# Kernel tuning notes

Hardware: AMD Instinct MI355X
Metric: run time of the kernel (lower is better)

Reference implementation:

```python
import jax, jax.numpy as jnp
import numpy as np

# dims: F=N_fault, V=N_train (noise samples), E=batch, M=n_in+2, N=n_out
F, V, E, N_IN, N_OUT = 2, 4, 2048, 512, 512
M = N_IN + 2
GMIN, GMAX, EPS_TRAIN, PGMIN = 0.01, 10.0, 0.1, 1e-4
ETA2_ACT1 = 0.20  # ACT1.eta_fault[0,2], used in theta init
# pTanh activation params per ACT: a = e0 + e1*tanh((z-e2)*e3)
ETAS = np.array([[0.05, 0.90, 0.20, 8.0],
                 [0.10, 0.80, 0.30, 5.0],
                 [0.00, 1.00, 0.25, 10.0],
                 [0.15, 0.70, 0.15, 6.0]], dtype=np.float32)


def setup_inputs() -> dict:
    key = jax.random.key(0)
    k1, k2, k3, k4, k5 = jax.random.split(key, 5)
    a_previous = jax.random.uniform(k1, (F, V, E, N_IN), jnp.float32)
    # theta init per __init__: rand/100 + gmin; last row += gmax; row -2 from eta_2 formula
    theta = jax.random.uniform(k2, (M, N_OUT), jnp.float32) / 100.0 + GMIN
    theta = theta.at[-1, :].add(GMAX)
    theta = theta.at[-2, :].set(ETA2_ACT1 / (1.0 - ETA2_ACT1) * (jnp.sum(theta[:-2, :], 0) + theta[-1, :]))
    cofficients_act = jax.random.uniform(k3, (4, N_OUT), jnp.float32)
    noise_u = jax.random.uniform(k4, (F, V, M, N_OUT), jnp.float32)   # theta_noisy uniform draw
    gumbel_u = jax.random.uniform(k5, (4, N_OUT), jnp.float32)        # gumbel uniform draw
    return {"a_previous": a_previous, "theta_": theta,
            "cofficients_act": cofficients_act, "noise_u": noise_u, "gumbel_u": gumbel_u}


def _forward(a_previous, theta_, cofficients_act, noise_u, gumbel_u):
    sg = jax.lax.stop_gradient
    # --- theta property: clamp to [-gmax,gmax], zero |.|<gmin, straight-through ---
    th_c = jnp.clip(theta_, -GMAX, GMAX)
    th_t = jnp.where(jnp.abs(th_c) < GMIN, 0.0, th_c)
    theta = sg(th_t) + theta_ - sg(theta_)
    # --- theta_noisy: multiplicative uniform noise in [1-eps, 1+eps]; FaultMask == 1 ---
    theta_noisy = theta[None, None] * ((noise_u * 2.0 - 1.0) * EPS_TRAIN + 1.0)  # [F,V,M,N]
    absn = jnp.abs(theta_noisy)
    W = absn / (jnp.sum(absn, axis=2, keepdims=True) + 1e-10)
    pos = (theta_noisy >= 0).astype(theta_noisy.dtype)
    neg = 1.0 - pos
    # --- MAC: extend input with [ones, zeros], inverter path, split-sign matmul ---
    ones = jnp.ones(a_previous.shape[:3] + (1,), a_previous.dtype)
    zeros = jnp.zeros_like(ones)
    x_ext = jnp.concatenate([a_previous, ones, zeros], axis=3)  # [F,V,E,M]
    x_neg = (-x_ext).at[..., -1].set(0.0)                       # ideal INV(a) = -a, last col zeroed
    z = (jnp.einsum('fvem,fvmn->fven', x_ext, W * pos)
         + jnp.einsum('fvem,fvmn->fven', x_neg, W * neg))       # [F,V,E,N]
    # --- MAC_power: vectorized form of the quad loop ---
    # Power = sum_{f,v,m,n} g[m,n] * sum_e (x_ext*pos + x_neg*neg - y)^2 / (E*V*F)
    # pos*neg = 0, pos^2 = pos  =>  expand the square into einsum reductions.
    g_init = jnp.abs(th_c)
    g_tilde = g_init * (PGMIN / jnp.min(g_init, axis=0, keepdims=True))
    pos_d, neg_d = sg(pos), sg(neg)  # detached in torch source
    sx2 = jnp.einsum('fvem,fvem->fvm', x_ext, x_ext)
    sn2 = jnp.einsum('fvem,fvem->fvm', x_neg, x_neg)
    sy2 = jnp.einsum('fven,fven->fvn', z, z)
    C = jnp.einsum('fvem,fven->fvmn', x_ext, z)
    D = jnp.einsum('fvem,fven->fvmn', x_neg, z)
    p1 = (jnp.einsum('fvm,fvmn,mn->', sx2, pos_d, g_tilde)
          + jnp.einsum('fvm,fvmn,mn->', sn2, neg_d, g_tilde))
    p2 = -2.0 * (jnp.einsum('fvmn,fvmn,mn->', C, pos_d, g_tilde)
                 + jnp.einsum('fvmn,fvmn,mn->', D, neg_d, g_tilde))
    p3 = jnp.einsum('fvn,n->', sy2, jnp.sum(g_tilde, axis=0))
    mac_power = (p1 + p2 + p3) / (E * V * F)
    # --- CoFF_ACT: clamped logits + gumbel, softmax, hard argmax straight-through ---
    c = cofficients_act + sg(jnp.clip(cofficients_act, -1.0, 1.0) - cofficients_act)
    gn = -jnp.log(-jnp.log(gumbel_u + 1e-20) + 1e-20)
    alpha = jax.nn.softmax((c + gn) / 1.0, axis=0)              # temperature = 1.0
    hard = jax.nn.one_hot(jnp.argmax(alpha, axis=0), 4, axis=0, dtype=alpha.dtype)
    alpha_st = sg(hard) + alpha - sg(alpha)                      # [4, N]
    # --- mix the four pTanh activations ---
    a_new = jnp.zeros_like(z)
    for i in range(4):
        e0, e1, e2, e3 = ETAS[i]
        a_new = a_new + alpha_st[i] * (e0 + e1 * jnp.tanh((z - e2) * e3))
    return a_new, mac_power


def reference(a_previous, theta_, cofficients_act, noise_u, gumbel_u):
    return _forward(a_previous, theta_, cofficients_act, noise_u, gumbel_u)
```

## Files before the change

kernel.cpp:

```cpp
#include <hip/hip_runtime.h>

typedef unsigned short u16;
typedef __attribute__((ext_vector_type(8))) short short8;
typedef __attribute__((ext_vector_type(4))) float f32x4;

#define NF 2
#define NV 4
#define FV 8
#define NE 2048
#define NIN 512
#define NOUT 512
#define NM 514

#define WS_P1      0u
#define WS_P2      2048u
#define WS_P3      3072u
#define WS_SCALE   4224u
#define WS_G       6272u
#define WS_GN      8448u
#define WS_ETA     10496u
#define WS_BIASZ   18688u
#define WS_BIAST   35072u
#define WS_DENP    51456u
#define WS_PMIN    182528u
#define WS_PSUM    313600u
#define WS_ABF     444672u
#define WS_BZT     17221888u
#define WS_BTT     21416192u

__constant__ float c_etas[4][4] = {
    {0.05f, 0.90f, 0.20f, 8.0f},
    {0.10f, 0.80f, 0.30f, 5.0f},
    {0.00f, 1.00f, 0.25f, 10.0f},
    {0.15f, 0.70f, 0.15f, 6.0f}};

__device__ __forceinline__ u16 f2bf(float x) {
    unsigned u = __float_as_uint(x);
    unsigned r = (u + 0x7fffu + ((u >> 16) & 1u)) >> 16;
    return (u16)r;
}

__device__ __forceinline__ void gll16(const void* g, void* l) {
    __builtin_amdgcn_global_load_lds((__attribute__((address_space(1))) void*)g,
                                     (__attribute__((address_space(3))) void*)l,
                                     16, 0, 0);
}

__global__ void kA_part(const float* __restrict__ theta_, float* __restrict__ pmin,
                        float* __restrict__ psum, float* __restrict__ wszero) {
    int t = threadIdx.x;
    if (blockIdx.x == 0) {
        for (int i = t; i < 1056; i += 256) wszero[i] = 0.f;
    }
    int n2 = t * 2;
    int r0 = blockIdx.x * 9;
    float mn0 = 3.4e38f, mn1 = 3.4e38f, s0 = 0.f, s1 = 0.f;
    int rend = r0 + 9;
    if (rend > NM) rend = NM;
    for (int r = r0; r < rend; r++) {
        float2 v = *(const float2*)(theta_ + r * NOUT + n2);
        float a0 = fabsf(fminf(fmaxf(v.x, -10.f), 10.f));
        float a1 = fabsf(fminf(fmaxf(v.y, -10.f), 10.f));
        mn0 = fminf(mn0, a0); mn1 = fminf(mn1, a1);
        s0 += a0; s1 += a1;
    }
    *(float2*)(pmin + blockIdx.x * NOUT + n2) = make_float2(mn0, mn1);
    *(float2*)(psum + blockIdx.x * NOUT + n2) = make_float2(s0, s1);
}

__global__ void kB_fold(const float* __restrict__ pmin, const float* __restrict__ psum,
                        const float* __restrict__ coeff, const float* __restrict__ gumb,
                        float* __restrict__ scale, float* __restrict__ Gn,
                        float4* __restrict__ eta4) {
    int n = threadIdx.x;
    float mn = 3.4e38f, s = 0.f;
    for (int i = 0; i < 64; i++) {
        mn = fminf(mn, pmin[i * NOUT + n]);
        s += psum[i * NOUT + n];
    }
    float sc = 1e-4f / mn;
    scale[n] = sc;
    Gn[n] = sc * s;
    float best = -1e30f;
    int bi = 0;
    for (int i = 0; i < 4; i++) {
        float c = fminf(fmaxf(coeff[i * NOUT + n], -1.f), 1.f);
        float u = gumb[i * NOUT + n];
        float g = -logf(-logf(u + 1e-20f) + 1e-20f);
        float v = c + g;
        if (v > best) { best = v; bi = i; }
    }
    eta4[n] = make_float4(c_etas[bi][0], c_etas[bi][1], c_etas[bi][2], c_etas[bi][3]);
}

__global__ void kC_grow(const float* __restrict__ theta_, const float* __restrict__ scale,
                        float* __restrict__ G) {
    int m = blockIdx.x;
    int t = threadIdx.x;
    const float4* rowp = (const float4*)(theta_ + m * NOUT);
    const float4* scp = (const float4*)scale;
    float acc = 0.f;
#pragma unroll
    for (int i = 0; i < 2; i++) {
        float4 v = rowp[t * 2 + i];
        float4 s = scp[t * 2 + i];
        acc += fabsf(fminf(fmaxf(v.x, -10.f), 10.f)) * s.x
             + fabsf(fminf(fmaxf(v.y, -10.f), 10.f)) * s.y
             + fabsf(fminf(fmaxf(v.z, -10.f), 10.f)) * s.z
             + fabsf(fminf(fmaxf(v.w, -10.f), 10.f)) * s.w;
    }
    for (int off = 32; off > 0; off >>= 1) acc += __shfl_down(acc, off);
    if (t == 0) G[m] = acc;
}

__global__ void k_wmat3(const float* __restrict__ theta_, const float* __restrict__ scale,
                        const float* __restrict__ noise,
                        u16* __restrict__ BzT, u16* __restrict__ BtT,
                        float* __restrict__ bias_z, float* __restrict__ bias_t,
                        float* __restrict__ denomp) {
    const int nt = blockIdx.x, mt = blockIdx.y, fv = blockIdx.z;
    const int t = threadIdx.x;
    const int nq = t & 15, mr = t >> 4;
    const int nb = nt * 64 + nq * 4;
    __shared__ u16 Wl[64][72];
    __shared__ u16 Sl[64][72];
    __shared__ float4 red[16][17];
    float4 sc4 = *(const float4*)(scale + nb);
    float4 dacc = {0.f, 0.f, 0.f, 0.f};
#pragma unroll
    for (int i = 0; i < 4; i++) {
        int ml = mr + i * 16;
        int m = mt * 64 + ml;
        float4 th4 = *(const float4*)(theta_ + m * NOUT + nb);
        float4 no4 = *(const float4*)(noise + (fv * NM + m) * NOUT + nb);
        ushort4 wv, sv;
#define WCOMP(c, fld) { float fac = no4.c * 0.2f + 0.9f; \
                        float thc = fminf(fmaxf(th4.c, -10.f), 10.f); \
                        float gi = fabsf(thc); \
                        float tht = (gi < 0.01f) ? 0.f : thc; \
                        float th = tht * fac; \
                        wv.fld = f2bf(th); \
                        sv.fld = f2bf(((th >= 0.f) ? gi : -gi) * sc4.c); \
                        dacc.c += fabsf(th); }
        WCOMP(x, x) WCOMP(y, y) WCOMP(z, z) WCOMP(w, w)
#undef WCOMP
        *(ushort4*)(&Wl[ml][nq * 4]) = wv;
        *(ushort4*)(&Sl[ml][nq * 4]) = sv;
    }
    red[mr][nq] = dacc;
    __syncthreads();
    if (t < 16) {
        float4 s = red[0][t];
#pragma unroll
        for (int r = 1; r < 16; r++) {
            float4 v = red[r][t];
            s.x += v.x; s.y += v.y; s.z += v.z; s.w += v.w;
        }
        *(float4*)(denomp + (mt * 8 + fv) * NOUT + nt * 64 + t * 4) = s;
    }
    const int mb = (t & 15) * 4;
#pragma unroll
    for (int r = 0; r < 4; r++) {
        int nl = (t >> 4) + r * 16;
        ushort4 wv, sv;
        wv.x = Wl[mb][nl]; wv.y = Wl[mb + 1][nl]; wv.z = Wl[mb + 2][nl]; wv.w = Wl[mb + 3][nl];
        sv.x = Sl[mb][nl]; sv.y = Sl[mb + 1][nl]; sv.z = Sl[mb + 2][nl]; sv.w = Sl[mb + 3][nl];
        int gidx = (fv * NOUT + nt * 64 + nl) * NIN + mt * 64 + mb;
        *(ushort4*)(BzT + gidx) = wv;
        *(ushort4*)(BtT + gidx) = sv;
    }
    if (mt == 0 && t < 64) {
        int n = nt * 64 + t;
        float fac = noise[(fv * NM + 512) * NOUT + n] * 0.2f + 0.9f;
        float thc = fminf(fmaxf(theta_[512 * NOUT + n], -10.f), 10.f);
        float gi = fabsf(thc);
        float tht = (gi < 0.01f) ? 0.f : thc;
        float th = tht * fac;
        bias_z[fv * NOUT + n] = th;
        bias_t[fv * NOUT + n] = ((th >= 0.f) ? gi : -gi) * scale[n];
    }
}

__global__ void k_prepA(const float* __restrict__ a_prev, const float* __restrict__ G,
                        u16* __restrict__ Abf, float* __restrict__ p1slot) {
    int t = threadIdx.x;
    float acc = 0.f;
#pragma unroll
    for (int i = 0; i < 4; i++) {
        int idx = (i * 2048 + blockIdx.x) * 256 + t;
        float4 v = ((const float4*)a_prev)[idx];
        int k = (idx & 127) << 2;
        float4 g4 = *((const float4*)(G + k));
        acc += v.x * v.x * g4.x + v.y * v.y * g4.y + v.z * v.z * g4.z + v.w * v.w * g4.w;
        ushort4 o;
        o.x = f2bf(v.x); o.y = f2bf(v.y); o.z = f2bf(v.z); o.w = f2bf(v.w);
        ((ushort4*)Abf)[idx] = o;
    }
    for (int off = 32; off > 0; off >>= 1) acc += __shfl_down(acc, off);
    __shared__ float red[4];
    int lane = t & 63, wv = t >> 6;
    if (lane == 0) red[wv] = acc;
    __syncthreads();
    if (t == 0)
        atomicAdd(&p1slot[(blockIdx.x & 63) * 8], red[0] + red[1] + red[2] + red[3]);
}

__global__ __launch_bounds__(256, 2) void k_gemm(
    const u16* __restrict__ Abf, const u16* __restrict__ BzT, const u16* __restrict__ BtT,
    const float* __restrict__ bias_z, const float* __restrict__ bias_t,
    const float* __restrict__ Gn, const float4* __restrict__ eta4,
    const float* __restrict__ theta_, const float* __restrict__ noise,
    const float* __restrict__ denomp,
    float* __restrict__ out, float* __restrict__ p2slot, float* __restrict__ p3slot) {
    __shared__ alignas(16) u16 As[128 * 64];
    __shared__ alignas(16) u16 Bzs[128 * 64];
    __shared__ alignas(16) u16 Bts[128 * 64];
    const int tid = threadIdx.x;
    const int lane = tid & 63;
    const int wv = tid >> 6;
    const int wr = wv >> 1, wc = wv & 1;
    const int b = blockIdx.x;
    const int fv = b & 7;
    const int kk = b >> 3;
    const int n0 = (kk & 3) * 128;
    const int e0 = (kk >> 2) * 128;

    const u16* Ag = Abf + (fv * NE + e0) * NIN;
    const u16* Bzg = BzT + (fv * NOUT + n0) * NIN;
    const u16* Btg = BtT + (fv * NOUT + n0) * NIN;

    f32x4 accz[4][4], acct[4][4];
#pragma unroll
    for (int i = 0; i < 4; i++)
#pragma unroll
        for (int j = 0; j < 4; j++) {
            f32x4 zz = {0.f, 0.f, 0.f, 0.f};
            accz[i][j] = zz;
            acct[i][j] = zz;
        }

    const int srow = tid >> 3;
    const int swz = (((tid & 7) ^ (srow & 7))) * 8;

    for (int k0 = 0; k0 < 512; k0 += 64) {
#pragma unroll
        for (int i = 0; i < 4; i++) {
            int so = (i * 32 + srow) * 512 + k0 + swz;
            int dof = i * 2048 + tid * 8;
            gll16(Ag + so, (u16*)As + dof);
            gll16(Bzg + so, (u16*)Bzs + dof);
            gll16(Btg + so, (u16*)Bts + dof);
        }
        __builtin_amdgcn_s_waitcnt(0);
        __syncthreads();
        const int rA = wr * 64 + (lane & 15);
        const int rB = wc * 64 + (lane & 15);
#pragma unroll
        for (int s = 0; s < 2; s++) {
            const int ca = ((s * 4 + (lane >> 4)) ^ (lane & 7)) * 8;
            short8 af[4], bzf[4], btf[4];
#pragma unroll
            for (int i = 0; i < 4; i++) af[i] = *(const short8*)(As + (rA + i * 16) * 64 + ca);
#pragma unroll
            for (int j = 0; j < 4; j++) {
                bzf[j] = *(const short8*)(Bzs + (rB + j * 16) * 64 + ca);
                btf[j] = *(const short8*)(Bts + (rB + j * 16) * 64 + ca);
            }
#pragma unroll
            for (int i = 0; i < 4; i++)
#pragma unroll
                for (int j = 0; j < 4; j++) {
                    accz[i][j] = __builtin_amdgcn_mfma_f32_16x16x32_bf16(af[i], bzf[j], accz[i][j], 0, 0, 0);
                    acct[i][j] = __builtin_amdgcn_mfma_f32_16x16x32_bf16(af[i], btf[j], acct[i][j], 0, 0, 0);
                }
        }
        __syncthreads();
    }

    float p2 = 0.f, p3 = 0.f;
    const int col = lane & 15;
    const int rowq = (lane >> 4) * 4;
#pragma unroll
    for (int j = 0; j < 4; j++) {
        int n = n0 + wc * 64 + j * 16 + col;
        float dsum = 1e-10f;
#pragma unroll
        for (int mc = 0; mc < 8; mc++) dsum += denomp[(mc * 8 + fv) * NOUT + n];
#pragma unroll
        for (int mx = 512; mx < 514; mx++) {
            float fac = noise[(fv * NM + mx) * NOUT + n] * 0.2f + 0.9f;
            float thc = fminf(fmaxf(theta_[mx * NOUT + n], -10.f), 10.f);
            float tht = (fabsf(thc) < 0.01f) ? 0.f : thc;
            dsum += fabsf(tht * fac);
        }
        float rdv = 1.f / dsum;
        float bz = bias_z[fv * NOUT + n];
        float bt = bias_t[fv * NOUT + n];
        float gnv = Gn[n];
        float4 e4 = eta4[n];
#pragma unroll
        for (int i = 0; i < 4; i++) {
            int ebase = e0 + wr * 64 + i * 16 + rowq;
#pragma unroll
            for (int r = 0; r < 4; r++) {
                float z = (accz[i][j][r] + bz) * rdv;
                float t = acct[i][j][r] + bt;
                p2 += z * t;
                p3 += z * z * gnv;
                float x = (z - e4.z) * e4.w;
                float ex = __expf(2.f * x);
                float th = 1.f - 2.f / (ex + 1.f);
                out[(fv * NE + ebase + r) * NOUT + n] = e4.x + e4.y * th;
            }
        }
    }
    for (int off = 32; off > 0; off >>= 1) {
        p2 += __shfl_down(p2, off);
        p3 += __shfl_down(p3, off);
    }
    __shared__ float r2[4], r3[4];
    if (lane == 0) { r2[wv] = p2; r3[wv] = p3; }
    __syncthreads();
    if (tid == 0) {
        int slot = (b & 31) * 8;
        atomicAdd(&p2slot[slot], r2[0] + r2[1] + r2[2] + r2[3]);
        atomicAdd(&p3slot[slot], r3[0] + r3[1] + r3[2] + r3[3]);
    }
}

__global__ void k_final(const float* __restrict__ p1s, const float* __restrict__ p2s,
                        const float* __restrict__ p3s, const float* __restrict__ G,
                        float* __restrict__ out) {
    int t = threadIdx.x;
    float s1 = p1s[t * 8];
    float s2 = (t < 32) ? p2s[t * 8] : 0.f;
    float s3 = (t < 32) ? p3s[t * 8] : 0.f;
    for (int off = 32; off > 0; off >>= 1) {
        s1 += __shfl_down(s1, off);
        s2 += __shfl_down(s2, off);
        s3 += __shfl_down(s3, off);
    }
    if (t == 0) {
        float mp = (s1 + 16384.f * G[512] - 2.f * s2 + s3) * (1.f / 16384.f);
        out[8388608] = mp;
    }
}

extern "C" void kernel_launch(void* const* d_in, const int* in_sizes, int n_in,
                              void* d_out, int out_size, void* d_ws, size_t ws_size,
                              hipStream_t stream) {
    const float* a_prev = (const float*)d_in[0];
    const float* theta_ = (const float*)d_in[1];
    const float* coeff = (const float*)d_in[2];
    const float* noise = (const float*)d_in[3];
    const float* gumb = (const float*)d_in[4];
    float* out = (float*)d_out;
    char* w = (char*)d_ws;
    float* p1s = (float*)(w + WS_P1);
    float* p2s = (float*)(w + WS_P2);
    float* p3s = (float*)(w + WS_P3);
    float* scale = (float*)(w + WS_SCALE);
    float* G = (float*)(w + WS_G);
    float* Gn = (float*)(w + WS_GN);
    float4* eta4 = (float4*)(w + WS_ETA);
    float* bias_z = (float*)(w + WS_BIASZ);
    float* bias_t = (float*)(w + WS_BIAST);
    float* denomp = (float*)(w + WS_DENP);
    float* pmin = (float*)(w + WS_PMIN);
    float* psum = (float*)(w + WS_PSUM);
    u16* Abf = (u16*)(w + WS_ABF);
    u16* BzT = (u16*)(w + WS_BZT);
    u16* BtT = (u16*)(w + WS_BTT);

    kA_part<<<64, 256, 0, stream>>>(theta_, pmin, psum, (float*)w);
    kB_fold<<<1, 512, 0, stream>>>(pmin, psum, coeff, gumb, scale, Gn, eta4);
    kC_grow<<<514, 64, 0, stream>>>(theta_, scale, G);
    k_wmat3<<<dim3(8, 8, FV), 256, 0, stream>>>(theta_, scale, noise, BzT, BtT,
                                                bias_z, bias_t, denomp);
    k_prepA<<<2048, 256, 0, stream>>>(a_prev, G, Abf, p1s);
    k_gemm<<<512, 256, 0, stream>>>(Abf, BzT, BtT, bias_z, bias_t, Gn, eta4,
                                    theta_, noise, denomp, out, p2s, p3s);
    k_final<<<1, 64, 0, stream>>>(p1s, p2s, p3s, G, out);
}
```

Baseline: 138.7 us.

## Double-buffer GEMM tiles with larger 128x256 blocks and fuse G row sums into wmat

The GEMM now uses 512-thread blocks covering 128x256 output tiles. It stages the next K tile into a second LDS buffer (160KB of dynamic shared memory) while computing on the current one, so global loads overlap with MFMA work. The separate kC_grow kernel is removed: the per-row G sums are accumulated with atomics inside k_wmat3 (only for fv==0), and the workspace zeroing is widened to cover G. kA_part uses fewer, larger blocks, and kB_fold folds 16 partials instead of 64. The large LDS footprint limits occupancy to one block per CU, and the atomics make G accumulation order nondeterministic.

```diff
diff --git a/kernel.cpp b/kernel.cpp
--- a/kernel.cpp
+++ b/kernel.cpp
@@ -50,12 +50,12 @@
                         float* __restrict__ psum, float* __restrict__ wszero) {
     int t = threadIdx.x;
     if (blockIdx.x == 0) {
-        for (int i = t; i < 1056; i += 256) wszero[i] = 0.f;
+        for (int i = t; i < 2112; i += 256) wszero[i] = 0.f;
     }
     int n2 = t * 2;
-    int r0 = blockIdx.x * 9;
+    int r0 = blockIdx.x * 33;
     float mn0 = 3.4e38f, mn1 = 3.4e38f, s0 = 0.f, s1 = 0.f;
-    int rend = r0 + 9;
+    int rend = r0 + 33;
     if (rend > NM) rend = NM;
     for (int r = r0; r < rend; r++) {
         float2 v = *(const float2*)(theta_ + r * NOUT + n2);
@@ -74,7 +74,8 @@
                         float4* __restrict__ eta4) {
     int n = threadIdx.x;
     float mn = 3.4e38f, s = 0.f;
-    for (int i = 0; i < 64; i++) {
+#pragma unroll
+    for (int i = 0; i < 16; i++) {
         mn = fminf(mn, pmin[i * NOUT + n]);
         s += psum[i * NOUT + n];
     }
@@ -93,31 +94,11 @@
     eta4[n] = make_float4(c_etas[bi][0], c_etas[bi][1], c_etas[bi][2], c_etas[bi][3]);
 }
 
-__global__ void kC_grow(const float* __restrict__ theta_, const float* __restrict__ scale,
-                        float* __restrict__ G) {
-    int m = blockIdx.x;
-    int t = threadIdx.x;
-    const float4* rowp = (const float4*)(theta_ + m * NOUT);
-    const float4* scp = (const float4*)scale;
-    float acc = 0.f;
-#pragma unroll
-    for (int i = 0; i < 2; i++) {
-        float4 v = rowp[t * 2 + i];
-        float4 s = scp[t * 2 + i];
-        acc += fabsf(fminf(fmaxf(v.x, -10.f), 10.f)) * s.x
-             + fabsf(fminf(fmaxf(v.y, -10.f), 10.f)) * s.y
-             + fabsf(fminf(fmaxf(v.z, -10.f), 10.f)) * s.z
-             + fabsf(fminf(fmaxf(v.w, -10.f), 10.f)) * s.w;
-    }
-    for (int off = 32; off > 0; off >>= 1) acc += __shfl_down(acc, off);
-    if (t == 0) G[m] = acc;
-}
-
 __global__ void k_wmat3(const float* __restrict__ theta_, const float* __restrict__ scale,
                         const float* __restrict__ noise,
                         u16* __restrict__ BzT, u16* __restrict__ BtT,
                         float* __restrict__ bias_z, float* __restrict__ bias_t,
-                        float* __restrict__ denomp) {
+                        float* __restrict__ denomp, float* __restrict__ G) {
     const int nt = blockIdx.x, mt = blockIdx.y, fv = blockIdx.z;
     const int t = threadIdx.x;
     const int nq = t & 15, mr = t >> 4;
@@ -134,6 +115,7 @@
         float4 th4 = *(const float4*)(theta_ + m * NOUT + nb);
         float4 no4 = *(const float4*)(noise + (fv * NM + m) * NOUT + nb);
         ushort4 wv, sv;
+        float gs = 0.f;
 #define WCOMP(c, fld) { float fac = no4.c * 0.2f + 0.9f; \
                         float thc = fminf(fmaxf(th4.c, -10.f), 10.f); \
                         float gi = fabsf(thc); \
@@ -141,11 +123,19 @@
                         float th = tht * fac; \
                         wv.fld = f2bf(th); \
                         sv.fld = f2bf(((th >= 0.f) ? gi : -gi) * sc4.c); \
+                        gs += gi * sc4.c; \
                         dacc.c += fabsf(th); }
         WCOMP(x, x) WCOMP(y, y) WCOMP(z, z) WCOMP(w, w)
 #undef WCOMP
         *(ushort4*)(&Wl[ml][nq * 4]) = wv;
         *(ushort4*)(&Sl[ml][nq * 4]) = sv;
+        if (fv == 0) {
+            gs += __shfl_xor(gs, 1);
+            gs += __shfl_xor(gs, 2);
+            gs += __shfl_xor(gs, 4);
+            gs += __shfl_xor(gs, 8);
+            if (nq == 0) atomicAdd(&G[m], gs);
+        }
     }
     red[mr][nq] = dacc;
     __syncthreads();
@@ -178,6 +168,11 @@
         float th = tht * fac;
         bias_z[fv * NOUT + n] = th;
         bias_t[fv * NOUT + n] = ((th >= 0.f) ? gi : -gi) * scale[n];
+        if (fv == 0) {
+            float gsb = gi * scale[n];
+            for (int off = 32; off > 0; off >>= 1) gsb += __shfl_down(gsb, off);
+            if (t == 0) atomicAdd(&G[512], gsb);
+        }
     }
 }
 
@@ -205,25 +200,45 @@
         atomicAdd(&p1slot[(blockIdx.x & 63) * 8], red[0] + red[1] + red[2] + red[3]);
 }
 
-__global__ __launch_bounds__(256, 2) void k_gemm(
+__device__ __forceinline__ void stage_tile(const u16* __restrict__ Ag,
+                                           const u16* __restrict__ Bzg,
+                                           const u16* __restrict__ Btg,
+                                           u16* Asd, u16* Bzd, u16* Btd,
+                                           int k0, int tid) {
+    const int srow = tid >> 3;
+    const int swz = ((tid & 7) ^ (srow & 7)) * 8;
+    const int dof = tid * 8;
+#pragma unroll
+    for (int i = 0; i < 2; i++)
+        gll16(Ag + (i * 64 + srow) * 512 + k0 + swz, Asd + i * 4096 + dof);
+#pragma unroll
+    for (int i = 0; i < 4; i++) {
+        int so = (i * 64 + srow) * 512 + k0 + swz;
+        gll16(Bzg + so, Bzd + i * 4096 + dof);
+        gll16(Btg + so, Btd + i * 4096 + dof);
+    }
+}
+
+__global__ __launch_bounds__(512, 2) void k_gemm(
     const u16* __restrict__ Abf, const u16* __restrict__ BzT, const u16* __restrict__ BtT,
     const float* __restrict__ bias_z, const float* __restrict__ bias_t,
     const float* __restrict__ Gn, const float4* __restrict__ eta4,
     const float* __restrict__ theta_, const float* __restrict__ noise,
     const float* __restrict__ denomp,
     float* __restrict__ out, float* __restrict__ p2slot, float* __restrict__ p3slot) {
-    __shared__ alignas(16) u16 As[128 * 64];
-    __shared__ alignas(16) u16 Bzs[128 * 64];
-    __shared__ alignas(16) u16 Bts[128 * 64];
+    extern __shared__ char smem[];
+    u16* smemA = (u16*)smem;
+    u16* smemBz = (u16*)(smem + 32768);
+    u16* smemBt = (u16*)(smem + 98304);
     const int tid = threadIdx.x;
     const int lane = tid & 63;
     const int wv = tid >> 6;
-    const int wr = wv >> 1, wc = wv & 1;
+    const int wr = wv >> 2, wc = wv & 3;
     const int b = blockIdx.x;
     const int fv = b & 7;
     const int kk = b >> 3;
-    const int n0 = (kk & 3) * 128;
-    const int e0 = (kk >> 2) * 128;
+    const int n0 = (kk & 1) * 256;
+    const int e0 = (kk >> 1) * 128;
 
     const u16* Ag = Abf + (fv * NE + e0) * NIN;
     const u16* Bzg = BzT + (fv * NOUT + n0) * NIN;
@@ -239,32 +254,32 @@
             acct[i][j] = zz;
         }
 
-    const int srow = tid >> 3;
-    const int swz = (((tid & 7) ^ (srow & 7))) * 8;
-
+    stage_tile(Ag, Bzg, Btg, smemA, smemBz, smemBt, 0, tid);
+    __builtin_amdgcn_s_waitcnt(0);
+    __syncthreads();
+
+    const int rA = wr * 64 + (lane & 15);
+    const int rB = wc * 64 + (lane & 15);
+    int buf = 0;
     for (int k0 = 0; k0 < 512; k0 += 64) {
-#pragma unroll
-        for (int i = 0; i < 4; i++) {
-            int so = (i * 32 + srow) * 512 + k0 + swz;
-            int dof = i * 2048 + tid * 8;
-            gll16(Ag + so, (u16*)As + dof);
-            gll16(Bzg + so, (u16*)Bzs + dof);
-            gll16(Btg + so, (u16*)Bts + dof);
-        }
-        __builtin_amdgcn_s_waitcnt(0);
-        __syncthreads();
-        const int rA = wr * 64 + (lane & 15);
-        const int rB = wc * 64 + (lane & 15);
+        if (k0 < 448)
+            stage_tile(Ag, Bzg, Btg,
+                       smemA + (buf ^ 1) * 8192,
+                       smemBz + (buf ^ 1) * 16384,
+                       smemBt + (buf ^ 1) * 16384, k0 + 64, tid);
+        const u16* Asb = smemA + buf * 8192;
+        const u16* Bzb = smemBz + buf * 16384;
+        const u16* Btb = smemBt + buf * 16384;
 #pragma unroll
         for (int s = 0; s < 2; s++) {
             const int ca = ((s * 4 + (lane >> 4)) ^ (lane & 7)) * 8;
             short8 af[4], bzf[4], btf[4];
 #pragma unroll
-            for (int i = 0; i < 4; i++) af[i] = *(const short8*)(As + (rA + i * 16) * 64 + ca);
+            for (int i = 0; i < 4; i++) af[i] = *(const short8*)(Asb + (rA + i * 16) * 64 + ca);
 #pragma unroll
             for (int j = 0; j < 4; j++) {
-                bzf[j] = *(const short8*)(Bzs + (rB + j * 16) * 64 + ca);
-                btf[j] = *(const short8*)(Bts + (rB + j * 16) * 64 + ca);
+                bzf[j] = *(const short8*)(Bzb + (rB + j * 16) * 64 + ca);
+                btf[j] = *(const short8*)(Btb + (rB + j * 16) * 64 + ca);
             }
 #pragma unroll
             for (int i = 0; i < 4; i++)
@@ -274,7 +289,9 @@
                     acct[i][j] = __builtin_amdgcn_mfma_f32_16x16x32_bf16(af[i], btf[j], acct[i][j], 0, 0, 0);
                 }
         }
+        __builtin_amdgcn_s_waitcnt(0);
         __syncthreads();
+        buf ^= 1;
     }
 
     float p2 = 0.f, p3 = 0.f;
@@ -318,13 +335,17 @@
         p2 += __shfl_down(p2, off);
         p3 += __shfl_down(p3, off);
     }
-    __shared__ float r2[4], r3[4];
+    float* r2 = (float*)smem;
+    float* r3 = r2 + 8;
     if (lane == 0) { r2[wv] = p2; r3[wv] = p3; }
     __syncthreads();
     if (tid == 0) {
+        float s2 = 0.f, s3 = 0.f;
+#pragma unroll
+        for (int q = 0; q < 8; q++) { s2 += r2[q]; s3 += r3[q]; }
         int slot = (b & 31) * 8;
-        atomicAdd(&p2slot[slot], r2[0] + r2[1] + r2[2] + r2[3]);
-        atomicAdd(&p3slot[slot], r3[0] + r3[1] + r3[2] + r3[3]);
+        atomicAdd(&p2slot[slot], s2);
+        atomicAdd(&p3slot[slot], s3);
     }
 }
 
@@ -372,13 +393,19 @@
     u16* BzT = (u16*)(w + WS_BZT);
     u16* BtT = (u16*)(w + WS_BTT);
 
-    kA_part<<<64, 256, 0, stream>>>(theta_, pmin, psum, (float*)w);
+    static bool attr_done = false;
+    if (!attr_done) {
+        (void)hipFuncSetAttribute((const void*)k_gemm,
+                                  hipFuncAttributeMaxDynamicSharedMemorySize, 163840);
+        attr_done = true;
+    }
+
+    kA_part<<<16, 256, 0, stream>>>(theta_, pmin, psum, (float*)w);
     kB_fold<<<1, 512, 0, stream>>>(pmin, psum, coeff, gumb, scale, Gn, eta4);
-    kC_grow<<<514, 64, 0, stream>>>(theta_, scale, G);
     k_wmat3<<<dim3(8, 8, FV), 256, 0, stream>>>(theta_, scale, noise, BzT, BtT,
-                                                bias_z, bias_t, denomp);
+                                                bias_z, bias_t, denomp, G);
     k_prepA<<<2048, 256, 0, stream>>>(a_prev, G, Abf, p1s);
-    k_gemm<<<512, 256, 0, stream>>>(Abf, BzT, BtT, bias_z, bias_t, Gn, eta4,
-                                    theta_, noise, denomp, out, p2s, p3s);
+    k_gemm<<<256, 512, 163840, stream>>>(Abf, BzT, BtT, bias_z, bias_t, Gn, eta4,
+                                         theta_, noise, denomp, out, p2s, p3s);
     k_final<<<1, 64, 0, stream>>>(p1s, p2s, p3s, G, out);
 }
```

New measurement: 145.4 us. 4.8% more time.

## Fold scale/G/eta prep kernels into k_wmat3 with atomic G accumulation

Applied to the files above, without the earlier changes.

Removes the kB_fold and kC_grow launches. k_wmat3 now reduces the per-column min directly from 16 partial blocks (kA_part now uses 16 blocks of 33 rows) and computes the scale inline. It builds G through shuffle reductions plus atomicAdd into a zeroed workspace region, whose zeroing is widened to cover G. This cuts two kernel launches and the serial single-block fold. The cost is redundant pmin reads in every block, atomics on G, and a nondeterministic floating-point summation order.

```diff
diff --git a/kernel.cpp b/kernel.cpp
--- a/kernel.cpp
+++ b/kernel.cpp
@@ -50,12 +50,12 @@
                         float* __restrict__ psum, float* __restrict__ wszero) {
     int t = threadIdx.x;
     if (blockIdx.x == 0) {
-        for (int i = t; i < 1056; i += 256) wszero[i] = 0.f;
+        for (int i = t; i < 2112; i += 256) wszero[i] = 0.f;
     }
     int n2 = t * 2;
-    int r0 = blockIdx.x * 9;
+    int r0 = blockIdx.x * 33;
     float mn0 = 3.4e38f, mn1 = 3.4e38f, s0 = 0.f, s1 = 0.f;
-    int rend = r0 + 9;
+    int rend = r0 + 33;
     if (rend > NM) rend = NM;
     for (int r = r0; r < rend; r++) {
         float2 v = *(const float2*)(theta_ + r * NOUT + n2);
@@ -68,56 +68,14 @@
     *(float2*)(psum + blockIdx.x * NOUT + n2) = make_float2(s0, s1);
 }
 
-__global__ void kB_fold(const float* __restrict__ pmin, const float* __restrict__ psum,
+__global__ void k_wmat3(const float* __restrict__ theta_,
+                        const float* __restrict__ pmin, const float* __restrict__ psum,
                         const float* __restrict__ coeff, const float* __restrict__ gumb,
-                        float* __restrict__ scale, float* __restrict__ Gn,
-                        float4* __restrict__ eta4) {
-    int n = threadIdx.x;
-    float mn = 3.4e38f, s = 0.f;
-    for (int i = 0; i < 64; i++) {
-        mn = fminf(mn, pmin[i * NOUT + n]);
-        s += psum[i * NOUT + n];
-    }
-    float sc = 1e-4f / mn;
-    scale[n] = sc;
-    Gn[n] = sc * s;
-    float best = -1e30f;
-    int bi = 0;
-    for (int i = 0; i < 4; i++) {
-        float c = fminf(fmaxf(coeff[i * NOUT + n], -1.f), 1.f);
-        float u = gumb[i * NOUT + n];
-        float g = -logf(-logf(u + 1e-20f) + 1e-20f);
-        float v = c + g;
-        if (v > best) { best = v; bi = i; }
-    }
-    eta4[n] = make_float4(c_etas[bi][0], c_etas[bi][1], c_etas[bi][2], c_etas[bi][3]);
-}
-
-__global__ void kC_grow(const float* __restrict__ theta_, const float* __restrict__ scale,
-                        float* __restrict__ G) {
-    int m = blockIdx.x;
-    int t = threadIdx.x;
-    const float4* rowp = (const float4*)(theta_ + m * NOUT);
-    const float4* scp = (const float4*)scale;
-    float acc = 0.f;
-#pragma unroll
-    for (int i = 0; i < 2; i++) {
-        float4 v = rowp[t * 2 + i];
-        float4 s = scp[t * 2 + i];
-        acc += fabsf(fminf(fmaxf(v.x, -10.f), 10.f)) * s.x
-             + fabsf(fminf(fmaxf(v.y, -10.f), 10.f)) * s.y
-             + fabsf(fminf(fmaxf(v.z, -10.f), 10.f)) * s.z
-             + fabsf(fminf(fmaxf(v.w, -10.f), 10.f)) * s.w;
-    }
-    for (int off = 32; off > 0; off >>= 1) acc += __shfl_down(acc, off);
-    if (t == 0) G[m] = acc;
-}
-
-__global__ void k_wmat3(const float* __restrict__ theta_, const float* __restrict__ scale,
                         const float* __restrict__ noise,
                         u16* __restrict__ BzT, u16* __restrict__ BtT,
                         float* __restrict__ bias_z, float* __restrict__ bias_t,
-                        float* __restrict__ denomp) {
+                        float* __restrict__ denomp, float* __restrict__ G,
+                        float* __restrict__ Gn, float4* __restrict__ eta4) {
     const int nt = blockIdx.x, mt = blockIdx.y, fv = blockIdx.z;
     const int t = threadIdx.x;
     const int nq = t & 15, mr = t >> 4;
@@ -125,7 +83,14 @@
     __shared__ u16 Wl[64][72];
     __shared__ u16 Sl[64][72];
     __shared__ float4 red[16][17];
-    float4 sc4 = *(const float4*)(scale + nb);
+    float4 mn4 = {3.4e38f, 3.4e38f, 3.4e38f, 3.4e38f};
+#pragma unroll
+    for (int i = 0; i < 16; i++) {
+        float4 v = *(const float4*)(pmin + i * NOUT + nb);
+        mn4.x = fminf(mn4.x, v.x); mn4.y = fminf(mn4.y, v.y);
+        mn4.z = fminf(mn4.z, v.z); mn4.w = fminf(mn4.w, v.w);
+    }
+    float4 sc4 = {1e-4f / mn4.x, 1e-4f / mn4.y, 1e-4f / mn4.z, 1e-4f / mn4.w};
     float4 dacc = {0.f, 0.f, 0.f, 0.f};
 #pragma unroll
     for (int i = 0; i < 4; i++) {
@@ -134,6 +99,7 @@
         float4 th4 = *(const float4*)(theta_ + m * NOUT + nb);
         float4 no4 = *(const float4*)(noise + (fv * NM + m) * NOUT + nb);
         ushort4 wv, sv;
+        float gs = 0.f;
 #define WCOMP(c, fld) { float fac = no4.c * 0.2f + 0.9f; \
                         float thc = fminf(fmaxf(th4.c, -10.f), 10.f); \
                         float gi = fabsf(thc); \
@@ -141,11 +107,19 @@
                         float th = tht * fac; \
                         wv.fld = f2bf(th); \
                         sv.fld = f2bf(((th >= 0.f) ? gi : -gi) * sc4.c); \
+                        gs += gi * sc4.c; \
                         dacc.c += fabsf(th); }
         WCOMP(x, x) WCOMP(y, y) WCOMP(z, z) WCOMP(w, w)
 #undef WCOMP
         *(ushort4*)(&Wl[ml][nq * 4]) = wv;
         *(ushort4*)(&Sl[ml][nq * 4]) = sv;
+        if (fv == 0) {
+            gs += __shfl_xor(gs, 1);
+            gs += __shfl_xor(gs, 2);
+            gs += __shfl_xor(gs, 4);
+            gs += __shfl_xor(gs, 8);
+            if (nq == 0) atomicAdd(&G[m], gs);
+        }
     }
     red[mr][nq] = dacc;
     __syncthreads();
@@ -171,13 +145,37 @@
     }
     if (mt == 0 && t < 64) {
         int n = nt * 64 + t;
+        float mn = 3.4e38f, s = 0.f;
+#pragma unroll
+        for (int i = 0; i < 16; i++) {
+            mn = fminf(mn, pmin[i * NOUT + n]);
+            s += psum[i * NOUT + n];
+        }
+        float sc = 1e-4f / mn;
         float fac = noise[(fv * NM + 512) * NOUT + n] * 0.2f + 0.9f;
         float thc = fminf(fmaxf(theta_[512 * NOUT + n], -10.f), 10.f);
         float gi = fabsf(thc);
         float tht = (gi < 0.01f) ? 0.f : thc;
         float th = tht * fac;
         bias_z[fv * NOUT + n] = th;
-        bias_t[fv * NOUT + n] = ((th >= 0.f) ? gi : -gi) * scale[n];
+        bias_t[fv * NOUT + n] = ((th >= 0.f) ? gi : -gi) * sc;
+        if (fv == 0) {
+            float gsb = gi * sc;
+            for (int off = 32; off > 0; off >>= 1) gsb += __shfl_down(gsb, off);
+            if (t == 0) atomicAdd(&G[512], gsb);
+        }
+        Gn[n] = sc * s;
+        float best = -1e30f;
+        int bi = 0;
+#pragma unroll
+        for (int i = 0; i < 4; i++) {
+            float c = fminf(fmaxf(coeff[i * NOUT + n], -1.f), 1.f);
+            float u = gumb[i * NOUT + n];
+            float g = -logf(-logf(u + 1e-20f) + 1e-20f);
+            float v = c + g;
+            if (v > best) { best = v; bi = i; }
+        }
+        eta4[n] = make_float4(c_etas[bi][0], c_etas[bi][1], c_etas[bi][2], c_etas[bi][3]);
     }
 }
 
@@ -359,7 +357,6 @@
     float* p1s = (float*)(w + WS_P1);
     float* p2s = (float*)(w + WS_P2);
     float* p3s = (float*)(w + WS_P3);
-    float* scale = (float*)(w + WS_SCALE);
     float* G = (float*)(w + WS_G);
     float* Gn = (float*)(w + WS_GN);
     float4* eta4 = (float4*)(w + WS_ETA);
@@ -372,11 +369,10 @@
     u16* BzT = (u16*)(w + WS_BZT);
     u16* BtT = (u16*)(w + WS_BTT);
 
-    kA_part<<<64, 256, 0, stream>>>(theta_, pmin, psum, (float*)w);
-    kB_fold<<<1, 512, 0, stream>>>(pmin, psum, coeff, gumb, scale, Gn, eta4);
-    kC_grow<<<514, 64, 0, stream>>>(theta_, scale, G);
-    k_wmat3<<<dim3(8, 8, FV), 256, 0, stream>>>(theta_, scale, noise, BzT, BtT,
-                                                bias_z, bias_t, denomp);
+    kA_part<<<16, 256, 0, stream>>>(theta_, pmin, psum, (float*)w);
+    k_wmat3<<<dim3(8, 8, FV), 256, 0, stream>>>(theta_, pmin, psum, coeff, gumb, noise,
+                                                BzT, BtT, bias_z, bias_t, denomp, G,
+                                                Gn, eta4);
     k_prepA<<<2048, 256, 0, stream>>>(a_prev, G, Abf, p1s);
     k_gemm<<<512, 256, 0, stream>>>(Abf, BzT, BtT, bias_z, bias_t, Gn, eta4,
                                     theta_, noise, denomp, out, p2s, p3s);
```

Result: no change. 138.9 us (+0.1%).
